# Kernel optimization log

Measured on AMD Instinct MI355X. Metric: run time of the kernel, lower is better.

## Reference

```python
import jax, jax.numpy as jnp
import numpy as np


def setup_inputs() -> dict:
    key = jax.random.key(0)
    k1, k2, k3 = jax.random.split(key, 3)
    N, E, D_IN, D_OUT = 100000, 1600000, 64, 64
    x = jax.random.normal(k1, (N, D_IN), dtype=jnp.float32)
    edge_index = jax.random.randint(k2, (2, E), 0, N, dtype=jnp.int64)
    # Glorot-style init for the GCN weight, zero bias (PyG defaults)
    W = jax.random.normal(k3, (D_IN, D_OUT), dtype=jnp.float32) * (1.0 / np.sqrt(D_IN))
    b = jnp.zeros((D_OUT,), dtype=jnp.float32)
    return {"x": x, "edge_index": edge_index, "W": W, "b": b}


def reference(x, edge_index, W, b):
    # GCNConv (PyG semantics, add_self_loops=True, normalize=True) followed by
    # Dropout (eval mode -> identity) and ReLU.
    N = x.shape[0]
    # Linear transform first (small GEMM)
    xw = x @ W  # [N, D_OUT]
    # Add self-loops
    loops = jnp.arange(N, dtype=edge_index.dtype)
    row = jnp.concatenate([edge_index[0], loops])  # source nodes
    col = jnp.concatenate([edge_index[1], loops])  # destination nodes
    # Symmetric degree normalization: deg over destination index (PyG gcn_norm)
    ones = jnp.ones(col.shape[0], dtype=xw.dtype)
    deg = jax.ops.segment_sum(ones, col, num_segments=N)
    deg_inv_sqrt = jnp.where(deg > 0, jax.lax.rsqrt(deg), 0.0)
    norm = deg_inv_sqrt[row] * deg_inv_sqrt[col]  # [E+N]
    # Gather source features, scale, scatter-add to destinations
    msgs = norm[:, None] * xw[row]  # [E+N, D_OUT]
    out = jax.ops.segment_sum(msgs, col, num_segments=N)
    out = out + b
    # dropout in eval mode is identity
    return jax.nn.relu(out)
```

## Files before the change

### kernel.cpp

```cpp
#include <hip/hip_runtime.h>
#include <hip/hip_fp16.h>


#define D 64
#define BW 256
#define CAPB 4800
#define CAPL2 4608
#define EPT 8
#define PART_T 512
#define EPB (PART_T * EPT)
#define NBMAX 512
#define GSTRIDE 16

typedef __attribute__((ext_vector_type(8))) short bf16x8;
typedef __attribute__((ext_vector_type(4))) float f32x4;

__device__ __forceinline__ unsigned short f2bf(float f) {
    unsigned u = __float_as_uint(f);
    u += 0x7FFFu + ((u >> 16) & 1u);
    return (unsigned short)(u >> 16);
}

__global__ __launch_bounds__(512, 4)
void k_part(const int* __restrict__ row, const int* __restrict__ col,
            int* __restrict__ gcur, int* __restrict__ dense,
            unsigned short* __restrict__ WT, const float* __restrict__ W,
            unsigned short* __restrict__ xw_h,
            int E, int NBUCK, int N) {
    __shared__ int lh[NBMAX];
    __shared__ int lst[NBMAX + 1];
    __shared__ int bas[NBMAX];
    __shared__ int wsc[8];
    __shared__ int srtv[EPB];
    __shared__ unsigned short srtb[EPB];
    int tid = threadIdx.x;
    for (int i = tid; i < NBUCK; i += PART_T) lh[i] = 0;
    __syncthreads();
    int e0 = blockIdx.x * EPB + tid;
    int rr[EPT], cc[EPT], pp[EPT];
#pragma unroll
    for (int i = 0; i < EPT; ++i) {
        int e = e0 + i * PART_T;
        if (e < E) {
            cc[i] = __builtin_nontemporal_load(col + e);
            rr[i] = __builtin_nontemporal_load(row + e);
            pp[i] = atomicAdd(&lh[cc[i] >> 8], 1);
        } else {
            cc[i] = -1;
        }
    }
    __syncthreads();
    int rot = (int)((blockIdx.x * 97u) % (unsigned)NBUCK);
    for (int j = tid; j < NBUCK; j += PART_T) {
        int bu = j + rot; if (bu >= NBUCK) bu -= NBUCK;
        int h = lh[bu];
        if (h > 0) bas[bu] = atomicAdd(&gcur[bu * GSTRIDE], h);
    }
    int lane = tid & 63, wv = tid >> 6;
    int v = (tid < NBUCK) ? lh[tid] : 0;
    int inc = v;
#pragma unroll
    for (int o = 1; o < 64; o <<= 1) {
        int u = __shfl_up(inc, o);
        if (lane >= o) inc += u;
    }
    if (lane == 63) wsc[wv] = inc;
    __syncthreads();
    int woff = 0;
#pragma unroll
    for (int w = 0; w < 8; ++w) woff += (w < wv) ? wsc[w] : 0;
    if (tid < NBUCK) lst[tid] = woff + inc - v;
    int tot = min(EPB, E - blockIdx.x * EPB);
    if (tid == 0) lst[NBUCK] = tot;
    __syncthreads();
#pragma unroll
    for (int i = 0; i < EPT; ++i) {
        if (cc[i] >= 0) {
            int bu = cc[i] >> 8;
            int pos = lst[bu] + pp[i];
            srtv[pos] = (rr[i] << 8) | (cc[i] & 255);
            srtb[pos] = (unsigned short)bu;
        }
    }
    __syncthreads();
    for (int p = tid; p < tot; p += PART_T) {
        int bu = srtb[p];
        int gpos = bas[bu] + (p - lst[bu]);
        if (gpos < CAPB) dense[(size_t)bu * CAPB + gpos] = srtv[p];
    }
    if (blockIdx.x == 0) {
        for (int i = tid; i < 4096; i += PART_T) {
            int n = i >> 6, k = i & 63;
            WT[i] = f2bf(W[k * 64 + n]);
        }
        if (tid < 32) ((unsigned*)xw_h)[(size_t)N * 32 + tid] = 0u;
    }
}

__global__ __launch_bounds__(256, 4)
void k_gemm(const float* __restrict__ x, const unsigned short* __restrict__ WT,
            const int* __restrict__ dense, const int* __restrict__ gcur,
            unsigned char* __restrict__ deg8, unsigned short* __restrict__ xw_h,
            int N, int NT) {
    __shared__ int lh[128];
    int tid = threadIdx.x, b2 = blockIdx.x;
    int bucket = b2 >> 1, hf = b2 & 1;
    int lane = tid & 63, wv = tid >> 6;
    int m = lane & 15, quad = lane >> 4;
    f32x4 xa[2][4];
#pragma unroll
    for (int s = 0; s < 2; ++s) {
        int mt = b2 * 8 + s * 4 + wv;
        if (mt < NT) {
            const float* xr = x + (size_t)(mt * 16 + m) * 64 + quad * 8;
            xa[s][0] = __builtin_nontemporal_load((const f32x4*)(xr));
            xa[s][1] = __builtin_nontemporal_load((const f32x4*)(xr + 4));
            xa[s][2] = __builtin_nontemporal_load((const f32x4*)(xr + 32));
            xa[s][3] = __builtin_nontemporal_load((const f32x4*)(xr + 36));
        }
    }
    if (tid < 128) lh[tid] = 0;
    __syncthreads();
    int tot = min(gcur[bucket * GSTRIDE], CAPB);
    const int* dn = dense + (size_t)bucket * CAPB;
    int hsel = hf << 7;
    for (int i = tid; i < tot; i += 256) {
        int val = __builtin_nontemporal_load(dn + i);
        if ((val & 128) == hsel) atomicAdd(&lh[val & 127], 1);
    }
    __syncthreads();
    if (tid < 128) {
        int node = b2 * 128 + tid;
        if (node < N) deg8[node] = (unsigned char)min(lh[tid], 255);
    }
    bf16x8 Bf[4][2];
#pragma unroll
    for (int t = 0; t < 4; ++t)
#pragma unroll
        for (int s = 0; s < 2; ++s)
            Bf[t][s] = *(const bf16x8*)(WT + (t * 16 + m) * 64 + s * 32 + quad * 8);
#pragma unroll
    for (int s = 0; s < 2; ++s) {
        int mt = b2 * 8 + s * 4 + wv;
        if (mt >= NT) continue;
        int row0 = mt * 16;
        bf16x8 A0, A1;
        A0[0] = (short)f2bf(xa[s][0][0]); A0[1] = (short)f2bf(xa[s][0][1]);
        A0[2] = (short)f2bf(xa[s][0][2]); A0[3] = (short)f2bf(xa[s][0][3]);
        A0[4] = (short)f2bf(xa[s][1][0]); A0[5] = (short)f2bf(xa[s][1][1]);
        A0[6] = (short)f2bf(xa[s][1][2]); A0[7] = (short)f2bf(xa[s][1][3]);
        A1[0] = (short)f2bf(xa[s][2][0]); A1[1] = (short)f2bf(xa[s][2][1]);
        A1[2] = (short)f2bf(xa[s][2][2]); A1[3] = (short)f2bf(xa[s][2][3]);
        A1[4] = (short)f2bf(xa[s][3][0]); A1[5] = (short)f2bf(xa[s][3][1]);
        A1[6] = (short)f2bf(xa[s][3][2]); A1[7] = (short)f2bf(xa[s][3][3]);
        f32x4 acc[4];
#pragma unroll
        for (int t = 0; t < 4; ++t) {
            acc[t] = (f32x4){0.f, 0.f, 0.f, 0.f};
            acc[t] = __builtin_amdgcn_mfma_f32_16x16x32_bf16(Bf[t][0], A0, acc[t], 0, 0, 0);
            acc[t] = __builtin_amdgcn_mfma_f32_16x16x32_bf16(Bf[t][1], A1, acc[t], 0, 0, 0);
        }
        float dsc = rsqrtf((float)(lh[(row0 + m) & 127] + 1));
        unsigned short* op = xw_h + (size_t)(row0 + m) * 64 + quad * 4;
#pragma unroll
        for (int t = 0; t < 4; ++t) {
            __half2 h0, h1;
            h0.x = __float2half(acc[t][0] * dsc); h0.y = __float2half(acc[t][1] * dsc);
            h1.x = __float2half(acc[t][2] * dsc); h1.y = __float2half(acc[t][3] * dsc);
            uint2 u; u.x = *(unsigned*)&h0; u.y = *(unsigned*)&h1;
            *(uint2*)(op + t * 16) = u;
        }
    }
}

__global__ __launch_bounds__(512, 6)
void k_gather(const int* __restrict__ dense, const int* __restrict__ gcur,
              const unsigned char* __restrict__ deg8,
              const uint4* __restrict__ xwh4, const float* __restrict__ bias,
              float* __restrict__ out, int N) {
    __shared__ int lh[128], stt[128], cur[128];
    __shared__ int wsum[2];
    __shared__ __align__(16) int srtL[CAPL2];
    int b2 = blockIdx.x, tid = threadIdx.x, lane = tid & 63;
    int bucket = b2 >> 1, hf = b2 & 1;
    int nb0 = b2 * 128;
    int v = 0, vp = 0, inc = 0;
    if (tid < 128) {
        int node = nb0 + tid;
        v = (node < N) ? (int)deg8[node] : 0;
        lh[tid] = v;
        vp = (v + 15) & ~15; inc = vp;
#pragma unroll
        for (int o = 1; o < 64; o <<= 1) {
            int u = __shfl_up(inc, o);
            if (lane >= o) inc += u;
        }
        if (lane == 63) wsum[tid >> 6] = inc;
    }
    __syncthreads();
    if (tid < 128) {
        int st = inc - vp + ((tid >> 6) ? wsum[0] : 0);
        stt[tid] = st;
        cur[tid] = st;
    }
    __syncthreads();
    int tot = min(gcur[bucket * GSTRIDE], CAPB);
    const int* dn = dense + (size_t)bucket * CAPB;
    int hsel = hf << 7;
    for (int i = tid; i < tot; i += 512) {
        int val = __builtin_nontemporal_load(dn + i);
        if ((val & 128) == hsel) {
            int pos = atomicAdd(&cur[val & 127], 1);
            if (pos < CAPL2) srtL[pos] = val >> 8;
        }
    }
    __syncthreads();
    if (tid < 128) {
        int e = stt[tid] + v, ep = min(stt[tid] + vp, CAPL2);
        for (; e < ep; ++e) srtL[e] = N;
    }
    __syncthreads();
    int q = lane >> 3;
    int l = lane & 7;
    int wv = tid >> 6;
    const float4 b0 = ((const float4*)bias)[2 * l];
    const float4 b1 = ((const float4*)bias)[2 * l + 1];
#define ADDV16(u)                                                     \
    {                                                                 \
        __half2 p0 = *(__half2*)&(u).x, p1 = *(__half2*)&(u).y;       \
        __half2 p2 = *(__half2*)&(u).z, p3 = *(__half2*)&(u).w;       \
        float2 f0 = __half22float2(p0), f1 = __half22float2(p1);      \
        float2 f2 = __half22float2(p2), f3 = __half22float2(p3);      \
        accA.x += f0.x; accA.y += f0.y; accA.z += f1.x; accA.w += f1.y;\
        accB.x += f2.x; accB.y += f2.y; accB.z += f3.x; accB.w += f3.y;\
    }
    for (int nn = wv * 16; nn < wv * 16 + 16; ++nn) {
        int node = nb0 + nn;
        if (node >= N) break;
        int k = lh[nn], s0 = stt[nn];
        int kp = (k + 15) & ~15;
        if (s0 + kp > CAPL2) kp = (CAPL2 > s0) ? ((CAPL2 - s0) & ~15) : 0;
        float4 accA = make_float4(0.f, 0.f, 0.f, 0.f);
        float4 accB = make_float4(0.f, 0.f, 0.f, 0.f);
        if (q == 0) { uint4 hs = xwh4[(size_t)node * 8 + l]; ADDV16(hs); }
        int rounds = kp >> 4;
        if (rounds > 0) {
            int i0 = s0 + q;
            int r0 = srtL[i0], r1 = srtL[i0 + 8];
            uint4 va = xwh4[(size_t)r0 * 8 + l];
            uint4 vb = xwh4[(size_t)r1 * 8 + l];
            for (int r = 1; r < rounds; ++r) {
                i0 += 16;
                int n0 = srtL[i0], n1 = srtL[i0 + 8];
                uint4 wa = xwh4[(size_t)n0 * 8 + l];
                uint4 wb = xwh4[(size_t)n1 * 8 + l];
                ADDV16(va); ADDV16(vb);
                va = wa; vb = wb;
            }
            ADDV16(va); ADDV16(vb);
        }
#pragma unroll
        for (int mm = 8; mm < 64; mm <<= 1) {
            accA.x += __shfl_xor(accA.x, mm); accA.y += __shfl_xor(accA.y, mm);
            accA.z += __shfl_xor(accA.z, mm); accA.w += __shfl_xor(accA.w, mm);
            accB.x += __shfl_xor(accB.x, mm); accB.y += __shfl_xor(accB.y, mm);
            accB.z += __shfl_xor(accB.z, mm); accB.w += __shfl_xor(accB.w, mm);
        }
        if (q == 0) {
            float dn2 = rsqrtf((float)(k + 1));
            f32x4 o1, o2;
            o1[0] = fmaxf(fmaf(dn2, accA.x, b0.x), 0.f);
            o1[1] = fmaxf(fmaf(dn2, accA.y, b0.y), 0.f);
            o1[2] = fmaxf(fmaf(dn2, accA.z, b0.z), 0.f);
            o1[3] = fmaxf(fmaf(dn2, accA.w, b0.w), 0.f);
            o2[0] = fmaxf(fmaf(dn2, accB.x, b1.x), 0.f);
            o2[1] = fmaxf(fmaf(dn2, accB.y, b1.y), 0.f);
            o2[2] = fmaxf(fmaf(dn2, accB.z, b1.z), 0.f);
            o2[3] = fmaxf(fmaf(dn2, accB.w, b1.w), 0.f);
            float* op = out + (size_t)node * 64 + l * 8;
            __builtin_nontemporal_store(o1, (f32x4*)op);
            __builtin_nontemporal_store(o2, (f32x4*)(op + 4));
        }
    }
#undef ADDV16
}

extern "C" void kernel_launch(void* const* d_in, const int* in_sizes, int n_in,
                              void* d_out, int out_size, void* d_ws, size_t ws_size,
                              hipStream_t stream) {
    const float* x    = (const float*)d_in[0];
    const int*   ei   = (const int*)d_in[1];
    const float* W    = (const float*)d_in[2];
    const float* bias = (const float*)d_in[3];
    float* out = (float*)d_out;

    const int N = in_sizes[0] / D;
    const int E = in_sizes[1] / 2;
    const int* row = ei;
    const int* col = ei + E;

    const int NBUCK = (N + BW - 1) / BW;
    const int NB1   = (E + EPB - 1) / EPB;
    const int NT    = (N + 15) / 16;
    const int NH    = 2 * NBUCK;

    char* ws = (char*)d_ws;
    size_t o = 0;
    unsigned short* xw_h = (unsigned short*)(ws + o);
    o += (size_t)(N + 1) * D * sizeof(unsigned short);
    int* dense = (int*)(ws + o); o += (size_t)NBUCK * CAPB * sizeof(int);
    int* gcur  = (int*)(ws + o); o += (size_t)NBUCK * GSTRIDE * sizeof(int);
    unsigned char* deg8 = (unsigned char*)(ws + o); o += (size_t)N;
    o = (o + 15) & ~(size_t)15;
    unsigned short* WT = (unsigned short*)(ws + o); o += 4096 * sizeof(unsigned short);

    hipMemsetAsync(gcur, 0, (size_t)NBUCK * GSTRIDE * sizeof(int), stream);
    k_part<<<NB1, PART_T, 0, stream>>>(row, col, gcur, dense, WT, W, xw_h, E, NBUCK, N);
    k_gemm<<<NH, 256, 0, stream>>>(x, WT, dense, gcur, deg8, xw_h, N, NT);
    k_gather<<<NH, 512, 0, stream>>>(dense, gcur, deg8, (const uint4*)xw_h,
                                     bias, out, N);
}
```

Measured before the change: 169.2 us.

## Gather one full 256-node bucket per 1024-thread block instead of half-buckets

The gather kernel now processes an entire destination bucket per block using 1024 threads, rather than two blocks each scanning the whole bucket's edge list and keeping only their half. This stops every dense bucket entry from being read twice and removes the half-select filter. The local sort buffer grows to hold a full bucket, padding is spread across four threads per node, and the wave-offset scan now spans four waves. In exchange the grid is half as large with bigger blocks and more shared memory each, which can reduce occupancy and load balance.

```diff
diff --git a/kernel.cpp b/kernel.cpp
--- a/kernel.cpp
+++ b/kernel.cpp
@@ -5,7 +5,7 @@
 #define D 64
 #define BW 256
 #define CAPB 4800
-#define CAPL2 4608
+#define CAPL 6912
 #define EPT 8
 #define PART_T 512
 #define EPB (PART_T * EPT)
@@ -173,20 +173,18 @@
     }
 }
 
-__global__ __launch_bounds__(512, 6)
+__global__ __launch_bounds__(1024, 8)
 void k_gather(const int* __restrict__ dense, const int* __restrict__ gcur,
               const unsigned char* __restrict__ deg8,
               const uint4* __restrict__ xwh4, const float* __restrict__ bias,
               float* __restrict__ out, int N) {
-    __shared__ int lh[128], stt[128], cur[128];
-    __shared__ int wsum[2];
-    __shared__ __align__(16) int srtL[CAPL2];
-    int b2 = blockIdx.x, tid = threadIdx.x, lane = tid & 63;
-    int bucket = b2 >> 1, hf = b2 & 1;
-    int nb0 = b2 * 128;
+    __shared__ int lh[BW], stt[BW], cur[BW];
+    __shared__ int wsum[4];
+    __shared__ __align__(16) int srtL[CAPL];
+    int b = blockIdx.x, tid = threadIdx.x, lane = tid & 63;
     int v = 0, vp = 0, inc = 0;
-    if (tid < 128) {
-        int node = nb0 + tid;
+    if (tid < BW) {
+        int node = b * BW + tid;
         v = (node < N) ? (int)deg8[node] : 0;
         lh[tid] = v;
         vp = (v + 15) & ~15; inc = vp;
@@ -198,26 +196,29 @@
         if (lane == 63) wsum[tid >> 6] = inc;
     }
     __syncthreads();
-    if (tid < 128) {
-        int st = inc - vp + ((tid >> 6) ? wsum[0] : 0);
+    if (tid < BW) {
+        int wv4 = tid >> 6, woff = 0;
+#pragma unroll
+        for (int w = 0; w < 4; ++w) woff += (w < wv4) ? wsum[w] : 0;
+        int st = woff + inc - vp;
         stt[tid] = st;
         cur[tid] = st;
     }
     __syncthreads();
-    int tot = min(gcur[bucket * GSTRIDE], CAPB);
-    const int* dn = dense + (size_t)bucket * CAPB;
-    int hsel = hf << 7;
-    for (int i = tid; i < tot; i += 512) {
+    int tot = min(gcur[b * GSTRIDE], CAPB);
+    const int* dn = dense + (size_t)b * CAPB;
+    for (int i = tid; i < tot; i += 1024) {
         int val = __builtin_nontemporal_load(dn + i);
-        if ((val & 128) == hsel) {
-            int pos = atomicAdd(&cur[val & 127], 1);
-            if (pos < CAPL2) srtL[pos] = val >> 8;
-        }
-    }
-    __syncthreads();
-    if (tid < 128) {
-        int e = stt[tid] + v, ep = min(stt[tid] + vp, CAPL2);
-        for (; e < ep; ++e) srtL[e] = N;
+        int pos = atomicAdd(&cur[val & 255], 1);
+        if (pos < CAPL) srtL[pos] = val >> 8;
+    }
+    __syncthreads();
+    {
+        int nn = tid >> 2, j = tid & 3;
+        int vv = lh[nn];
+        int e0p = stt[nn] + vv + j;
+        int ep = min(stt[nn] + ((vv + 15) & ~15), CAPL);
+        for (int e = e0p; e < ep; e += 4) srtL[e] = N;
     }
     __syncthreads();
     int q = lane >> 3;
@@ -235,11 +236,11 @@
         accB.x += f2.x; accB.y += f2.y; accB.z += f3.x; accB.w += f3.y;\
     }
     for (int nn = wv * 16; nn < wv * 16 + 16; ++nn) {
-        int node = nb0 + nn;
+        int node = b * BW + nn;
         if (node >= N) break;
         int k = lh[nn], s0 = stt[nn];
         int kp = (k + 15) & ~15;
-        if (s0 + kp > CAPL2) kp = (CAPL2 > s0) ? ((CAPL2 - s0) & ~15) : 0;
+        if (s0 + kp > CAPL) kp = (CAPL > s0) ? ((CAPL - s0) & ~15) : 0;
         float4 accA = make_float4(0.f, 0.f, 0.f, 0.f);
         float4 accB = make_float4(0.f, 0.f, 0.f, 0.f);
         if (q == 0) { uint4 hs = xwh4[(size_t)node * 8 + l]; ADDV16(hs); }
@@ -317,6 +318,6 @@
     hipMemsetAsync(gcur, 0, (size_t)NBUCK * GSTRIDE * sizeof(int), stream);
     k_part<<<NB1, PART_T, 0, stream>>>(row, col, gcur, dense, WT, W, xw_h, E, NBUCK, N);
     k_gemm<<<NH, 256, 0, stream>>>(x, WT, dense, gcur, deg8, xw_h, N, NT);
-    k_gather<<<NH, 512, 0, stream>>>(dense, gcur, deg8, (const uint4*)xw_h,
-                                     bias, out, N);
-}
+    k_gather<<<NBUCK, 1024, 0, stream>>>(dense, gcur, deg8, (const uint4*)xw_h,
+                                         bias, out, N);
+}
```

New measurement: 167.8 us. No clear change (-0.8%).
